# Optimization experiments

Measured on AMD Instinct MI355X. Metric: run time of the kernel, lower is better.

The kernel has to match this reference:

```python
import jax, jax.numpy as jnp
import numpy as np

N, IN_FEATS, HIDDEN, N_CLASSES = 12000, 256, 256, 40
EPS = 1e-12  # F.normalize default eps


def setup_inputs() -> dict:
    key = jax.random.key(0)
    ks = jax.random.split(key, 6)
    # dense adjacency, scaled like a row-normalized graph operator
    adj = jax.random.uniform(ks[0], (N, N), jnp.float32) * (1.0 / 64.0)
    x = jax.random.normal(ks[1], (N, IN_FEATS), jnp.float32)
    # xavier-uniform-like weights, zero biases (matches init_params)
    def xavier(k, fan_in, fan_out):
        lim = np.sqrt(6.0 / (fan_in + fan_out)).astype(np.float32)
        return jax.random.uniform(k, (fan_in, fan_out), jnp.float32, -lim, lim)
    W0 = xavier(ks[2], IN_FEATS, HIDDEN)
    W1 = xavier(ks[3], HIDDEN, HIDDEN)
    W2 = xavier(ks[4], HIDDEN, N_CLASSES)
    b0 = jnp.zeros((HIDDEN,), jnp.float32)
    b1 = jnp.zeros((HIDDEN,), jnp.float32)
    b2 = jnp.zeros((N_CLASSES,), jnp.float32)
    return {"adj": adj, "x": x, "W0": W0, "b0": b0, "W1": W1, "b1": b1, "W2": W2, "b2": b2}


def _l2_normalize(h):
    # F.normalize(h): rows divided by max(||row||_2, eps)
    norm = jnp.sqrt(jnp.sum(h * h, axis=1, keepdims=True))
    return h / jnp.maximum(norm, EPS)


def reference(adj, x, W0, b0, W1, b1, W2, b2):
    # layer 0: aggregate -> linear -> bias -> relu -> l2-normalize (dropout=eval identity)
    h = _l2_normalize(jax.nn.relu((adj @ x) @ W0 + b0))
    # layer 1 (hidden)
    h = _l2_normalize(jax.nn.relu((adj @ h) @ W1 + b1))
    # output layer: no activation / normalize / dropout
    h = (adj @ h) @ W2 + b2
    return h
```

## Files before the change

kernel.cpp:

```cpp
#include <hip/hip_runtime.h>
#include <hip/hip_bf16.h>

#define M_ROWS 12000
#define K_PAD  12032
#define FEAT   256
#define NCLS   40
#define NSLICE 5
#define NTILES 188
#define NBM    47
#define PSLABE (M_ROWS * FEAT)
#define TILE_SHORTS 16384
#define HALF_SHORTS 8192

typedef __attribute__((ext_vector_type(4))) float f32x4;
typedef __attribute__((ext_vector_type(8))) short s16x8;
typedef __attribute__((ext_vector_type(4))) short s16x4;
typedef unsigned int u32;

__device__ __forceinline__ short f2bf(float f){
  __hip_bfloat16 h = __float2bfloat16(f);
  union { __hip_bfloat16 h; short s; } u; u.h = h; return u.s;
}
__device__ __forceinline__ float bf2f(short s){
  union { float f; u32 u; } v; v.u = ((u32)(unsigned short)s) << 16; return v.f;
}

__device__ __forceinline__ f32x4 mfma16(s16x8 a, s16x8 b, f32x4 c){
  return __builtin_amdgcn_mfma_f32_16x16x32_bf16(a, b, c, 0, 0, 0);
}

__device__ __forceinline__ void gl16(const void* g, void* l){
  __builtin_amdgcn_global_load_lds(
      (const __attribute__((address_space(1))) u32*)g,
      (__attribute__((address_space(3))) u32*)l, 16, 0, 0);
}

#define VM6   do { asm volatile("s_waitcnt vmcnt(6)" ::: "memory"); \
                   __builtin_amdgcn_sched_barrier(0); } while(0)
#define VM4   do { asm volatile("s_waitcnt vmcnt(4)" ::: "memory"); \
                   __builtin_amdgcn_sched_barrier(0); } while(0)
#define VM0   do { asm volatile("s_waitcnt vmcnt(0)" ::: "memory"); \
                   __builtin_amdgcn_sched_barrier(0); } while(0)
#define LGK0  do { asm volatile("s_waitcnt lgkmcnt(0)" ::: "memory"); \
                   __builtin_amdgcn_sched_barrier(0); } while(0)
#define BARR  do { __builtin_amdgcn_s_barrier(); \
                   __builtin_amdgcn_sched_barrier(0); } while(0)

__device__ __forceinline__ int swz(int r){ return (r & 3) ^ ((r >> 2) & 3); }

__global__ __launch_bounds__(256) void k_transpose_pack(const float* __restrict__ src,
                                                        short* __restrict__ Bpack){
  const int t = threadIdx.x;
  if (blockIdx.x == 375){
    short* d = Bpack + (size_t)187 * TILE_SHORTS + HALF_SHORTS + t * 32;
    s16x8 z = (s16x8)0;
    #pragma unroll
    for (int i = 0; i < 4; ++i) *(s16x8*)(d + 8*i) = z;
    return;
  }
  __shared__ float tile[32][257];
  const int r0 = blockIdx.x * 32;
  {
    const int r = t >> 3, cs = (t & 7) * 32;
    const float* s = src + (size_t)(r0 + r) * FEAT + cs;
    #pragma unroll
    for (int i = 0; i < 8; ++i){
      f32x4 v = *(const f32x4*)(s + 4*i);
      tile[r][cs + 4*i + 0] = v[0];
      tile[r][cs + 4*i + 1] = v[1];
      tile[r][cs + 4*i + 2] = v[2];
      tile[r][cs + 4*i + 3] = v[3];
    }
  }
  __syncthreads();
  const int c = t;
  const int kt = r0 >> 6, hh = (r0 >> 5) & 1, sc = swz(c);
  short* d = Bpack + (size_t)kt * TILE_SHORTS + hh * HALF_SHORTS + c * 32;
  #pragma unroll
  for (int i = 0; i < 4; ++i){
    s16x8 o;
    #pragma unroll
    for (int j = 0; j < 8; ++j) o[j] = f2bf(tile[8*i + j][c]);
    *(s16x8*)(d + ((i ^ sc) * 8)) = o;
  }
}

__global__ __launch_bounds__(512, 2) void k_gemm_l0(const float* __restrict__ adj,
                                                    const short* __restrict__ Bpack,
                                                    short* __restrict__ Apack,
                                                    short* __restrict__ Pbase){
  __shared__ __align__(16) short lds[2][4][8192];

  const int t = threadIdx.x;
  const int w = t >> 6, l = t & 63;
  const int wm = w >> 2, wn = w & 3;
  const int lr = l & 15, lg = l >> 4;

  int id = blockIdx.x;
  {
    const int xcd = id & 7, idx = id >> 3;
    id = (xcd < 3 ? xcd * 30 : 90 + (xcd - 3) * 29) + idx;
  }
  const int bm = id % NBM, s = id / NBM;
  const int row0 = bm * 256;
  const int u0  = (s < 3) ? s * 38 : 114 + (s - 3) * 37;
  const int nst = (s < 3) ? 38 : 37;

  const char* Bb = (const char*)Bpack;
  const size_t tp = (size_t)t * 16;
  short* Aw = Apack + (size_t)bm * NTILES * TILE_SHORTS;

  size_t abase[2];
  #pragma unroll
  for (int p = 0; p < 2; ++p){
    const int si = p * 512 + t;
    const int r  = si >> 2, sl = si & 3;
    int grow = row0 + r; if (grow > M_ROWS - 1) grow = M_ROWS - 1;
    abase[p] = (size_t)grow * M_ROWS + (size_t)((sl ^ swz(r)) * 8);
  }

  f32x4 av0[4], av1[4];

#define ISSUE_A0(kt) do{ \
    av0[0] = *(const f32x4*)(adj + abase[0] + (kt)*64);      \
    av0[1] = *(const f32x4*)(adj + abase[0] + (kt)*64 + 4);  \
    av0[2] = *(const f32x4*)(adj + abase[1] + (kt)*64);      \
    av0[3] = *(const f32x4*)(adj + abase[1] + (kt)*64 + 4); }while(0)
#define ISSUE_A1(kt) do{ \
    av1[0] = *(const f32x4*)(adj + abase[0] + (kt)*64 + 32);     \
    av1[1] = *(const f32x4*)(adj + abase[0] + (kt)*64 + 32 + 4); \
    av1[2] = *(const f32x4*)(adj + abase[1] + (kt)*64 + 32);     \
    av1[3] = *(const f32x4*)(adj + abase[1] + (kt)*64 + 32 + 4); }while(0)

#define CVT_WRITE_A(q, h, kt, AV) do{                                         \
    _Pragma("unroll")                                                         \
    for (int p = 0; p < 2; ++p){                                              \
      s16x8 o;                                                                \
      _Pragma("unroll")                                                       \
      for (int j = 0; j < 4; ++j){ o[j] = f2bf(AV[2*p][j]); o[4+j] = f2bf(AV[2*p+1][j]); } \
      const int si = p * 512 + t;                                             \
      *(s16x8*)&lds[q][h][si * 8] = o;                                        \
      *(s16x8*)(Aw + (size_t)(kt) * TILE_SHORTS + (h) * HALF_SHORTS + si * 8) = o; \
    } }while(0)

#define ST_BH(q, h, kt) do{                                                   \
    const char* s_ = Bb + (size_t)(kt) * 32768 + (h) * 16384 + tp;            \
    gl16(s_,        (char*)&lds[q][2+(h)][0] + w*1024);                       \
    gl16(s_ + 8192, (char*)&lds[q][2+(h)][0] + 8192 + w*1024); }while(0)

#define AF(q, h, mf) \
    (*(const s16x8*)&lds[q][h][ (wm*128 + (mf)*16 + lr) * 32 + \
      ((lg ^ swz(wm*128 + (mf)*16 + lr)) * 8) ])
#define BF(q, h, nf) \
    (*(const s16x8*)&lds[q][2+(h)][ (wn*64 + (nf)*16 + lr) * 32 + \
      ((lg ^ swz(wn*64 + (nf)*16 + lr)) * 8) ])

  f32x4 acc[8][4];
  #pragma unroll
  for (int m = 0; m < 8; ++m)
    #pragma unroll
    for (int n = 0; n < 4; ++n) acc[m][n] = (f32x4)(0.0f);

  ISSUE_A0(u0); ST_BH(0, 0, u0);
  ISSUE_A1(u0); ST_BH(0, 1, u0);
  VM6;  CVT_WRITE_A(0, 0, u0, av0);
  VM0;  CVT_WRITE_A(0, 1, u0, av1);
  LGK0;
  BARR;

  for (int t2 = 0; t2 < nst; ++t2){
    const int q = t2 & 1, qn = q ^ 1;
    const bool stg = (t2 + 1 < nst);
    const int ktn = u0 + t2 + 1;

    s16x8 bfr[4], af[4];

    #pragma unroll
    for (int n = 0; n < 4; ++n) bfr[n] = BF(q, 0, n);
    #pragma unroll
    for (int m = 0; m < 4; ++m) af[m] = AF(q, 0, m);
    if (stg){ ISSUE_A0(ktn); ST_BH(qn, 0, ktn); }
    BARR;
    __builtin_amdgcn_s_setprio(1);
    #pragma unroll
    for (int m = 0; m < 4; ++m)
      #pragma unroll
      for (int n = 0; n < 4; ++n)
        acc[m][n] = mfma16(af[m], bfr[n], acc[m][n]);
    __builtin_amdgcn_s_setprio(0);
    BARR;

    #pragma unroll
    for (int m = 0; m < 4; ++m) af[m] = AF(q, 0, m + 4);
    if (stg){ ISSUE_A1(ktn); ST_BH(qn, 1, ktn); }
    BARR;
    __builtin_amdgcn_s_setprio(1);
    #pragma unroll
    for (int m = 0; m < 4; ++m)
      #pragma unroll
      for (int n = 0; n < 4; ++n)
        acc[m + 4][n] = mfma16(af[m], bfr[n], acc[m + 4][n]);
    __builtin_amdgcn_s_setprio(0);
    BARR;

    #pragma unroll
    for (int n = 0; n < 4; ++n) bfr[n] = BF(q, 1, n);
    #pragma unroll
    for (int m = 0; m < 4; ++m) af[m] = AF(q, 1, m);
    if (stg){ VM6; CVT_WRITE_A(qn, 0, ktn, av0); }
    BARR;
    __builtin_amdgcn_s_setprio(1);
    #pragma unroll
    for (int m = 0; m < 4; ++m)
      #pragma unroll
      for (int n = 0; n < 4; ++n)
        acc[m][n] = mfma16(af[m], bfr[n], acc[m][n]);
    __builtin_amdgcn_s_setprio(0);
    BARR;

    #pragma unroll
    for (int m = 0; m < 4; ++m) af[m] = AF(q, 1, m + 4);
    if (stg){ VM0; CVT_WRITE_A(qn, 1, ktn, av1); }
    BARR;
    __builtin_amdgcn_s_setprio(1);
    #pragma unroll
    for (int m = 0; m < 4; ++m)
      #pragma unroll
      for (int n = 0; n < 4; ++n)
        acc[m + 4][n] = mfma16(af[m], bfr[n], acc[m + 4][n]);
    __builtin_amdgcn_s_setprio(0);
    if (stg) LGK0;
    BARR;
  }
#undef ISSUE_A0
#undef ISSUE_A1
#undef CVT_WRITE_A
#undef ST_BH
#undef AF
#undef BF

  short* P = Pbase + (size_t)s * PSLABE;
  #pragma unroll
  for (int m = 0; m < 8; ++m){
    const int row = row0 + wm*128 + m*16 + lg*4;
    #pragma unroll
    for (int n = 0; n < 4; ++n){
      const int col = wn*64 + n*16 + lr;
      short* pp = P + (size_t)row * FEAT + col;
      #pragma unroll
      for (int r = 0; r < 4; ++r)
        if (row + r < M_ROWS) pp[(size_t)r * FEAT] = f2bf(acc[m][n][r]);
    }
  }
}

__global__ __launch_bounds__(512, 2) void k_gemm8p(const short* __restrict__ Apack,
                                                   const short* __restrict__ Bpack,
                                                   short* __restrict__ Pbase){
  __shared__ __align__(16) short lds[2][4][8192];

  const int t = threadIdx.x;
  const int w = t >> 6, l = t & 63;
  const int wm = w >> 2, wn = w & 3;
  const int lr = l & 15, lg = l >> 4;

  int id = blockIdx.x;
  {
    const int xcd = id & 7, idx = id >> 3;
    id = (xcd < 3 ? xcd * 30 : 90 + (xcd - 3) * 29) + idx;
  }
  const int bm = id % NBM, s = id / NBM;
  const int row0 = bm * 256;
  const int u0  = (s < 3) ? s * 38 : 114 + (s - 3) * 37;
  const int nst = (s < 3) ? 38 : 37;

  const char* Ab = (const char*)(Apack + (size_t)bm * NTILES * TILE_SHORTS);
  const char* Bb = (const char*)Bpack;
  const size_t tp = (size_t)t * 16;

#define ST_AH(q, h, kt) do{                                                   \
    const char* s_ = Ab + (size_t)(kt) * 32768 + (h) * 16384 + tp;            \
    gl16(s_,        (char*)&lds[q][h][0] + w*1024);                           \
    gl16(s_ + 8192, (char*)&lds[q][h][0] + 8192 + w*1024); }while(0)
#define ST_BH(q, h, kt) do{                                                   \
    const char* s_ = Bb + (size_t)(kt) * 32768 + (h) * 16384 + tp;            \
    gl16(s_,        (char*)&lds[q][2+(h)][0] + w*1024);                       \
    gl16(s_ + 8192, (char*)&lds[q][2+(h)][0] + 8192 + w*1024); }while(0)

#define AF(q, h, mf) \
    (*(const s16x8*)&lds[q][h][ (wm*128 + (mf)*16 + lr) * 32 + \
      ((lg ^ swz(wm*128 + (mf)*16 + lr)) * 8) ])
#define BF(q, h, nf) \
    (*(const s16x8*)&lds[q][2+(h)][ (wn*64 + (nf)*16 + lr) * 32 + \
      ((lg ^ swz(wn*64 + (nf)*16 + lr)) * 8) ])

  f32x4 acc[8][4];
  #pragma unroll
  for (int m = 0; m < 8; ++m)
    #pragma unroll
    for (int n = 0; n < 4; ++n) acc[m][n] = (f32x4)(0.0f);

  ST_BH(0, 0, u0); ST_AH(0, 0, u0);
  ST_BH(0, 1, u0); ST_AH(0, 1, u0);
  VM4;
  BARR;

  for (int t2 = 0; t2 < nst; ++t2){
    const int q = t2 & 1, qn = q ^ 1;
    const bool stg = (t2 + 1 < nst);
    const int ktn = u0 + t2 + 1;

    s16x8 bfr[4], af[4];

    #pragma unroll
    for (int n = 0; n < 4; ++n) bfr[n] = BF(q, 0, n);
    #pragma unroll
    for (int m = 0; m < 4; ++m) af[m] = AF(q, 0, m);
    if (stg) ST_BH(qn, 0, ktn);
    BARR;
    __builtin_amdgcn_s_setprio(1);
    #pragma unroll
    for (int m = 0; m < 4; ++m)
      #pragma unroll
      for (int n = 0; n < 4; ++n)
        acc[m][n] = mfma16(af[m], bfr[n], acc[m][n]);
    __builtin_amdgcn_s_setprio(0);
    BARR;

    #pragma unroll
    for (int m = 0; m < 4; ++m) af[m] = AF(q, 0, m + 4);
    if (stg) ST_AH(qn, 0, ktn);
    BARR;
    __builtin_amdgcn_s_setprio(1);
    #pragma unroll
    for (int m = 0; m < 4; ++m)
      #pragma unroll
      for (int n = 0; n < 4; ++n)
        acc[m + 4][n] = mfma16(af[m], bfr[n], acc[m + 4][n]);
    __builtin_amdgcn_s_setprio(0);
    if (stg) { VM4; } else { VM0; }
    BARR;

    #pragma unroll
    for (int n = 0; n < 4; ++n) bfr[n] = BF(q, 1, n);
    #pragma unroll
    for (int m = 0; m < 4; ++m) af[m] = AF(q, 1, m);
    if (stg) ST_BH(qn, 1, ktn);
    BARR;
    __builtin_amdgcn_s_setprio(1);
    #pragma unroll
    for (int m = 0; m < 4; ++m)
      #pragma unroll
      for (int n = 0; n < 4; ++n)
        acc[m][n] = mfma16(af[m], bfr[n], acc[m][n]);
    __builtin_amdgcn_s_setprio(0);
    BARR;

    #pragma unroll
    for (int m = 0; m < 4; ++m) af[m] = AF(q, 1, m + 4);
    if (stg) ST_AH(qn, 1, ktn);
    BARR;
    __builtin_amdgcn_s_setprio(1);
    #pragma unroll
    for (int m = 0; m < 4; ++m)
      #pragma unroll
      for (int n = 0; n < 4; ++n)
        acc[m + 4][n] = mfma16(af[m], bfr[n], acc[m + 4][n]);
    __builtin_amdgcn_s_setprio(0);
    if (stg) { VM4; }
    BARR;
  }
#undef ST_AH
#undef ST_BH
#undef AF
#undef BF

  short* P = Pbase + (size_t)s * PSLABE;
  #pragma unroll
  for (int m = 0; m < 8; ++m){
    const int row = row0 + wm*128 + m*16 + lg*4;
    #pragma unroll
    for (int n = 0; n < 4; ++n){
      const int col = wn*64 + n*16 + lr;
      short* pp = P + (size_t)row * FEAT + col;
      #pragma unroll
      for (int r = 0; r < 4; ++r)
        if (row + r < M_ROWS) pp[(size_t)r * FEAT] = f2bf(acc[m][n][r]);
    }
  }
}

__global__ __launch_bounds__(256) void k_fused2(const short* __restrict__ Pb,
                                                const float* __restrict__ W,
                                                const float* __restrict__ b,
                                                short* __restrict__ Bpack){
  __shared__ float ylds[32][257];
  __shared__ float red[32][33];
  __shared__ float scale[32];
  const int t  = threadIdx.x;
  const int r0 = blockIdx.x * 32;
  {
    const int r = t >> 3, cs = (t & 7) * 32;
    const size_t off = (size_t)(r0 + r) * FEAT + cs;
    float aa[32];
    {
      const short* p0 = Pb + off;
      #pragma unroll
      for (int i4 = 0; i4 < 4; ++i4){
        s16x8 v = *(const s16x8*)(p0 + i4*8);
        #pragma unroll
        for (int e = 0; e < 8; ++e) aa[i4*8 + e] = bf2f(v[e]);
      }
    }
    #pragma unroll
    for (int s = 1; s < NSLICE; ++s){
      const short* ps = Pb + (size_t)s * PSLABE + off;
      #pragma unroll
      for (int i4 = 0; i4 < 4; ++i4){
        s16x8 v = *(const s16x8*)(ps + i4*8);
        #pragma unroll
        for (int e = 0; e < 8; ++e) aa[i4*8 + e] += bf2f(v[e]);
      }
    }
    #pragma unroll
    for (int k = 0; k < 32; ++k) ylds[r][cs + k] = aa[k];
  }
  __syncthreads();

  const int rg = t >> 5;
  const int cg = t & 31;
  float acc[4][8];
  {
    float bias[8];
    #pragma unroll
    for (int j = 0; j < 8; ++j) bias[j] = b[cg*8 + j];
    #pragma unroll
    for (int i = 0; i < 4; ++i)
      #pragma unroll
      for (int j = 0; j < 8; ++j) acc[i][j] = bias[j];
  }

  #pragma unroll 4
  for (int k = 0; k < FEAT; ++k){
    float yv[4];
    #pragma unroll
    for (int i = 0; i < 4; ++i) yv[i] = ylds[rg*4 + i][k];
    f32x4 w0 = *(const f32x4*)(W + (size_t)k * FEAT + cg*8);
    f32x4 w1 = *(const f32x4*)(W + (size_t)k * FEAT + cg*8 + 4);
    #pragma unroll
    for (int i = 0; i < 4; ++i){
      #pragma unroll
      for (int j = 0; j < 4; ++j){
        acc[i][j]     += yv[i] * w0[j];
        acc[i][4 + j] += yv[i] * w1[j];
      }
    }
  }

  #pragma unroll
  for (int i = 0; i < 4; ++i){
    float ss = 0.0f;
    #pragma unroll
    for (int j = 0; j < 8; ++j){
      float v = fmaxf(acc[i][j], 0.0f);
      acc[i][j] = v;
      ss += v * v;
    }
    red[rg*4 + i][cg] = ss;
  }
  __syncthreads();
  if (t < 32){
    float ssum = 0.0f;
    #pragma unroll
    for (int j = 0; j < 32; ++j) ssum += red[t][j];
    scale[t] = 1.0f / fmaxf(sqrtf(ssum), 1e-12f);
  }
  __syncthreads();

  float sc[4];
  #pragma unroll
  for (int i = 0; i < 4; ++i) sc[i] = scale[rg*4 + i];

  const int kb   = r0 + rg * 4;
  const int kt   = kb >> 6, hh = (kb >> 5) & 1, g = (kb >> 3) & 3, e0 = kb & 7;
  short* dbase = Bpack + (size_t)kt * TILE_SHORTS + hh * HALF_SHORTS;
  #pragma unroll
  for (int j = 0; j < 8; ++j){
    const int c = cg * 8 + j;
    s16x4 o;
    #pragma unroll
    for (int i = 0; i < 4; ++i) o[i] = f2bf(acc[i][j] * sc[i]);
    *(s16x4*)(dbase + c * 32 + ((g ^ swz(c)) * 8) + e0) = o;
  }
}

__global__ __launch_bounds__(256) void k_final2(const short* __restrict__ Pb,
                                                const float* __restrict__ W2,
                                                const float* __restrict__ b2,
                                                float* __restrict__ out){
  __shared__ float ylds[32][257];
  const int t  = threadIdx.x;
  const int r0 = blockIdx.x * 32;
  {
    const int r = t >> 3, cs = (t & 7) * 32;
    const size_t off = (size_t)(r0 + r) * FEAT + cs;
    float aa[32];
    {
      const short* p0 = Pb + off;
      #pragma unroll
      for (int i4 = 0; i4 < 4; ++i4){
        s16x8 v = *(const s16x8*)(p0 + i4*8);
        #pragma unroll
        for (int e = 0; e < 8; ++e) aa[i4*8 + e] = bf2f(v[e]);
      }
    }
    #pragma unroll
    for (int s = 1; s < NSLICE; ++s){
      const short* ps = Pb + (size_t)s * PSLABE + off;
      #pragma unroll
      for (int i4 = 0; i4 < 4; ++i4){
        s16x8 v = *(const s16x8*)(ps + i4*8);
        #pragma unroll
        for (int e = 0; e < 8; ++e) aa[i4*8 + e] += bf2f(v[e]);
      }
    }
    #pragma unroll
    for (int k = 0; k < 32; ++k) ylds[r][cs + k] = aa[k];
  }
  __syncthreads();

  #pragma unroll
  for (int e = t; e < 32 * NCLS; e += 256){
    const int r = e / NCLS, n = e % NCLS;
    float a = b2[n];
    #pragma unroll 8
    for (int k = 0; k < FEAT; ++k)
      a = fmaf(ylds[r][k], W2[(size_t)k * NCLS + n], a);
    out[(size_t)(r0 + r) * NCLS + n] = a;
  }
}

extern "C" void kernel_launch(void* const* d_in, const int* in_sizes, int n_in,
                              void* d_out, int out_size, void* d_ws, size_t ws_size,
                              hipStream_t stream){
  const float* adj = (const float*)d_in[0];
  const float* x   = (const float*)d_in[1];
  const float* W0  = (const float*)d_in[2];
  const float* b0  = (const float*)d_in[3];
  const float* W1  = (const float*)d_in[4];
  const float* b1  = (const float*)d_in[5];
  const float* W2  = (const float*)d_in[6];
  const float* b2  = (const float*)d_in[7];
  float* out = (float*)d_out;

  char* ws = (char*)d_ws;
  const size_t BPACK_BYTES = (size_t)NTILES * TILE_SHORTS * 2;
  const size_t APACK_BYTES = (size_t)NBM * NTILES * TILE_SHORTS * 2;

  short* Bpack = (short*)ws;
  short* Apack = (short*)(ws + BPACK_BYTES);
  short* P     = (short*)(ws + BPACK_BYTES + APACK_BYTES);

  const dim3 b256(256), b512(512);

  k_transpose_pack<<<376, b256, 0, stream>>>(x, Bpack);

  k_gemm_l0<<<NBM * NSLICE, b512, 0, stream>>>(adj, Bpack, Apack, P);
  k_fused2<<<375, b256, 0, stream>>>(P, W0, b0, Bpack);
  k_gemm8p<<<NBM * NSLICE, b512, 0, stream>>>(Apack, Bpack, P);
  k_fused2<<<375, b256, 0, stream>>>(P, W1, b1, Bpack);
  k_gemm8p<<<NBM * NSLICE, b512, 0, stream>>>(Apack, Bpack, P);
  k_final2<<<375, b256, 0, stream>>>(P, W2, b2, out);
}
```

Measured before the change: 501.5 us.

## Triple-buffer A tiles with two-step lookahead in aggregation GEMM

Replaces the double-buffered pack GEMM with a variant that keeps three A buffers and three B half-buffers in LDS. A tiles are prefetched two k-steps ahead and B halves one step ahead. The inner loop is restructured from four phases of 4x4 MFMAs to two phases of 8x4 MFMAs, halving the barrier count per k-step and hiding more global-load latency. In exchange it uses more LDS (144KB vs 128KB per block, with two blocks per CU requested) and more registers for the 8 A fragments, which may reduce occupancy.

```diff
diff --git a/kernel.cpp b/kernel.cpp
--- a/kernel.cpp
+++ b/kernel.cpp
@@ -45,6 +45,7 @@
                    __builtin_amdgcn_sched_barrier(0); } while(0)
 #define BARR  do { __builtin_amdgcn_s_barrier(); \
                    __builtin_amdgcn_sched_barrier(0); } while(0)
+#define SBAR  __builtin_amdgcn_sched_barrier(0)
 
 __device__ __forceinline__ int swz(int r){ return (r & 3) ^ ((r >> 2) & 3); }
 
@@ -254,10 +255,11 @@
   }
 }
 
-__global__ __launch_bounds__(512, 2) void k_gemm8p(const short* __restrict__ Apack,
-                                                   const short* __restrict__ Bpack,
-                                                   short* __restrict__ Pbase){
-  __shared__ __align__(16) short lds[2][4][8192];
+__global__ __launch_bounds__(512, 2) void k_gemm_la2(const short* __restrict__ Apack,
+                                                     const short* __restrict__ Bpack,
+                                                     short* __restrict__ Pbase){
+  __shared__ __align__(16) short Alds[3][16384];
+  __shared__ __align__(16) short Blds[3][8192];
 
   const int t = threadIdx.x;
   const int w = t >> 6, l = t & 63;
@@ -278,20 +280,20 @@
   const char* Bb = (const char*)Bpack;
   const size_t tp = (size_t)t * 16;
 
-#define ST_AH(q, h, kt) do{                                                   \
+#define ST_AH(buf, kt, h) do{                                                 \
     const char* s_ = Ab + (size_t)(kt) * 32768 + (h) * 16384 + tp;            \
-    gl16(s_,        (char*)&lds[q][h][0] + w*1024);                           \
-    gl16(s_ + 8192, (char*)&lds[q][h][0] + 8192 + w*1024); }while(0)
-#define ST_BH(q, h, kt) do{                                                   \
+    gl16(s_,        (char*)&Alds[buf][(h)*8192] + w*1024);                    \
+    gl16(s_ + 8192, (char*)&Alds[buf][(h)*8192] + 8192 + w*1024); }while(0)
+#define ST_BH(buf, kt, h) do{                                                 \
     const char* s_ = Bb + (size_t)(kt) * 32768 + (h) * 16384 + tp;            \
-    gl16(s_,        (char*)&lds[q][2+(h)][0] + w*1024);                       \
-    gl16(s_ + 8192, (char*)&lds[q][2+(h)][0] + 8192 + w*1024); }while(0)
-
-#define AF(q, h, mf) \
-    (*(const s16x8*)&lds[q][h][ (wm*128 + (mf)*16 + lr) * 32 + \
+    gl16(s_,        (char*)&Blds[buf][0] + w*1024);                           \
+    gl16(s_ + 8192, (char*)&Blds[buf][0] + 8192 + w*1024); }while(0)
+
+#define AF(buf, h, mf) \
+    (*(const s16x8*)&Alds[buf][ (h)*8192 + (wm*128 + (mf)*16 + lr) * 32 + \
       ((lg ^ swz(wm*128 + (mf)*16 + lr)) * 8) ])
-#define BF(q, h, nf) \
-    (*(const s16x8*)&lds[q][2+(h)][ (wn*64 + (nf)*16 + lr) * 32 + \
+#define BF(buf, nf) \
+    (*(const s16x8*)&Blds[buf][ (wn*64 + (nf)*16 + lr) * 32 + \
       ((lg ^ swz(wn*64 + (nf)*16 + lr)) * 8) ])
 
   f32x4 acc[8][4];
@@ -300,27 +302,31 @@
     #pragma unroll
     for (int n = 0; n < 4; ++n) acc[m][n] = (f32x4)(0.0f);
 
-  ST_BH(0, 0, u0); ST_AH(0, 0, u0);
-  ST_BH(0, 1, u0); ST_AH(0, 1, u0);
-  VM4;
+  ST_AH(0, u0, 0); ST_AH(0, u0, 1);
+  SBAR;
+  ST_BH(0, u0, 0); ST_BH(1, u0, 1);
+  SBAR;
+  if (nst > 1){ ST_AH(1, u0 + 1, 0); ST_AH(1, u0 + 1, 1); VM4; }
+  else        { VM0; }
   BARR;
 
   for (int t2 = 0; t2 < nst; ++t2){
-    const int q = t2 & 1, qn = q ^ 1;
-    const bool stg = (t2 + 1 < nst);
-    const int ktn = u0 + t2 + 1;
-
-    s16x8 bfr[4], af[4];
-
-    #pragma unroll
-    for (int n = 0; n < 4; ++n) bfr[n] = BF(q, 0, n);
-    #pragma unroll
-    for (int m = 0; m < 4; ++m) af[m] = AF(q, 0, m);
-    if (stg) ST_BH(qn, 0, ktn);
+    const int a0 = t2 % 3;
+    const int b0 = (2*t2) % 3, b1 = (2*t2 + 1) % 3;
+    const bool s1 = (t2 + 1 < nst), s2 = (t2 + 2 < nst);
+    const int kt1 = u0 + t2 + 1, kt2 = u0 + t2 + 2;
+
+    s16x8 bfr[4], af[8];
+
+    #pragma unroll
+    for (int n = 0; n < 4; ++n) bfr[n] = BF(b0, n);
+    #pragma unroll
+    for (int m = 0; m < 8; ++m) af[m] = AF(a0, 0, m);
+    if (s1) ST_BH((2*t2 + 2) % 3, kt1, 0);
     BARR;
     __builtin_amdgcn_s_setprio(1);
     #pragma unroll
-    for (int m = 0; m < 4; ++m)
+    for (int m = 0; m < 8; ++m)
       #pragma unroll
       for (int n = 0; n < 4; ++n)
         acc[m][n] = mfma16(af[m], bfr[n], acc[m][n]);
@@ -328,46 +334,22 @@
     BARR;
 
     #pragma unroll
-    for (int m = 0; m < 4; ++m) af[m] = AF(q, 0, m + 4);
-    if (stg) ST_AH(qn, 0, ktn);
+    for (int n = 0; n < 4; ++n) bfr[n] = BF(b1, n);
+    #pragma unroll
+    for (int m = 0; m < 8; ++m) af[m] = AF(a0, 1, m);
+    if (s1) ST_BH((2*t2 + 3) % 3, kt1, 1);
+    SBAR;
+    if (s2){ ST_AH((t2 + 2) % 3, kt2, 0); ST_AH((t2 + 2) % 3, kt2, 1); }
     BARR;
     __builtin_amdgcn_s_setprio(1);
     #pragma unroll
-    for (int m = 0; m < 4; ++m)
-      #pragma unroll
-      for (int n = 0; n < 4; ++n)
-        acc[m + 4][n] = mfma16(af[m], bfr[n], acc[m + 4][n]);
-    __builtin_amdgcn_s_setprio(0);
-    if (stg) { VM4; } else { VM0; }
-    BARR;
-
-    #pragma unroll
-    for (int n = 0; n < 4; ++n) bfr[n] = BF(q, 1, n);
-    #pragma unroll
-    for (int m = 0; m < 4; ++m) af[m] = AF(q, 1, m);
-    if (stg) ST_BH(qn, 1, ktn);
-    BARR;
-    __builtin_amdgcn_s_setprio(1);
-    #pragma unroll
-    for (int m = 0; m < 4; ++m)
+    for (int m = 0; m < 8; ++m)
       #pragma unroll
       for (int n = 0; n < 4; ++n)
         acc[m][n] = mfma16(af[m], bfr[n], acc[m][n]);
     __builtin_amdgcn_s_setprio(0);
-    BARR;
-
-    #pragma unroll
-    for (int m = 0; m < 4; ++m) af[m] = AF(q, 1, m + 4);
-    if (stg) ST_AH(qn, 1, ktn);
-    BARR;
-    __builtin_amdgcn_s_setprio(1);
-    #pragma unroll
-    for (int m = 0; m < 4; ++m)
-      #pragma unroll
-      for (int n = 0; n < 4; ++n)
-        acc[m + 4][n] = mfma16(af[m], bfr[n], acc[m + 4][n]);
-    __builtin_amdgcn_s_setprio(0);
-    if (stg) { VM4; }
+    if (s2)      { VM4; }
+    else if (s1) { VM0; }
     BARR;
   }
 #undef ST_AH
@@ -567,8 +549,8 @@
 
   k_gemm_l0<<<NBM * NSLICE, b512, 0, stream>>>(adj, Bpack, Apack, P);
   k_fused2<<<375, b256, 0, stream>>>(P, W0, b0, Bpack);
-  k_gemm8p<<<NBM * NSLICE, b512, 0, stream>>>(Apack, Bpack, P);
+  k_gemm_la2<<<NBM * NSLICE, b512, 0, stream>>>(Apack, Bpack, P);
   k_fused2<<<375, b256, 0, stream>>>(P, W1, b1, Bpack);
-  k_gemm8p<<<NBM * NSLICE, b512, 0, stream>>>(Apack, Bpack, P);
+  k_gemm_la2<<<NBM * NSLICE, b512, 0, stream>>>(Apack, Bpack, P);
   k_final2<<<375, b256, 0, stream>>>(P, W2, b2, out);
 }
```

New measurement: 526.8 us. 5.0% more time.
